# Performance work log

Measured on AMD Instinct MI355X. Metric: run time of the kernel, lower is better.

Reference implementation:

```python
import jax, jax.numpy as jnp
import numpy as np

BS, N, H = 8, 2048, 512
NEG_INF = -1.0e9
LEAKY_SLOPE = 0.01  # torch nn.LeakyReLU default


def setup_inputs() -> dict:
    key = jax.random.key(0)
    ks = jax.random.split(key, 8)
    feats = jax.random.normal(ks[0], (BS, N, H), dtype=jnp.float32)
    # random 0/1 adjacency with self-loops so every row has >=1 neighbor
    adj = jax.random.randint(ks[1], (BS, N, N), 0, 2).astype(jnp.float32)
    adj = jnp.maximum(adj, jnp.eye(N, dtype=jnp.float32)[None])
    s = 1.0 / np.sqrt(H)
    return {
        "feats": feats,
        "adj_mat": adj,
        "fc_w": jax.random.normal(ks[2], (H, H), dtype=jnp.float32) * s,
        "fc_b": jax.random.normal(ks[3], (H,), dtype=jnp.float32) * s,
        "q_w": jax.random.normal(ks[4], (1, H), dtype=jnp.float32) * s,
        "q_b": jax.random.normal(ks[5], (1,), dtype=jnp.float32) * s,
        "k_w": jax.random.normal(ks[6], (1, H), dtype=jnp.float32) * s,
        "k_b": jax.random.normal(ks[7], (1,), dtype=jnp.float32) * s,
    }


def reference(feats, adj_mat, fc_w, fc_b, q_w, q_b, k_w, k_b):
    # feats: [bs, N, H]; torch Linear: x @ W.T + b
    feat_proj = jnp.einsum("bnh,oh->bno", feats, fc_w) + fc_b          # [bs, N, H]
    q = jnp.einsum("bnh,oh->bno", feat_proj, q_w) + q_b                # [bs, N, 1]
    k = jnp.einsum("bnh,oh->bno", feat_proj, k_w) + k_b                # [bs, N, 1]
    logits = q + jnp.swapaxes(k, 2, 1)                                 # [bs, N, N] broadcast add
    masked = logits + (1.0 - adj_mat) * NEG_INF
    masked = jnp.where(masked >= 0, masked, LEAKY_SLOPE * masked)      # LeakyReLU
    atten = jax.nn.softmax(masked, axis=-1)
    # dropout is identity in eval mode
    out = jnp.einsum("bnm,bmh->bnh", atten, feat_proj)
    return out + feats  # residual=True
```

## Files before the change

kernel.cpp:

```cpp
#include <hip/hip_runtime.h>
#include <hip/hip_bf16.h>
#include <cstdint>
#include <cstddef>

#define BSZ 8
#define NN 2048
#define HH 512
#define MROWS (BSZ * NN)
#define LOG2E 1.44269504088896f

typedef __attribute__((ext_vector_type(4))) float f32x4;
typedef __attribute__((ext_vector_type(8))) short short8;
typedef __attribute__((ext_vector_type(4))) unsigned short us4;
typedef __attribute__((ext_vector_type(4))) uint32_t u32x4;

#if __has_builtin(__builtin_amdgcn_exp2f)
#define EXP2(x) __builtin_amdgcn_exp2f(x)
#else
#define EXP2(x) __expf((x) * 0.69314718056f)
#endif

static __device__ __forceinline__ unsigned short f2bf(float f) {
    uint32_t u = __builtin_bit_cast(uint32_t, f);
    u += 0x7fffu + ((u >> 16) & 1u);
    return (unsigned short)(u >> 16);
}

static __device__ __forceinline__ void async16(const unsigned short* g, unsigned short* l) {
    __builtin_amdgcn_global_load_lds(
        (const __attribute__((address_space(1))) void*)g,
        (__attribute__((address_space(3))) void*)l, 16, 0, 0);
}

__global__ __launch_bounds__(256) void prep_kernel(
    const float* __restrict__ feats, const float* __restrict__ fc_w,
    unsigned short* __restrict__ feats_bf, unsigned short* __restrict__ fcw_bf) {
    const int bid = blockIdx.x;
    const int tid = threadIdx.x;
    if (bid < 2048) {
        const int base = bid * 1024 + tid;
#pragma unroll
        for (int j = 0; j < 4; ++j) {
            const int i = base + j * 256;
            f32x4 v = ((const f32x4*)feats)[i];
            us4 o;
#pragma unroll
            for (int c = 0; c < 4; ++c) o[c] = f2bf(v[c]);
            ((us4*)feats_bf)[i] = o;
        }
    } else {
        const int base = (bid - 2048) * 1024 + tid;
#pragma unroll
        for (int j = 0; j < 4; ++j) {
            const int i = base + j * 256;
            f32x4 v = ((const f32x4*)fc_w)[i];
            us4 o;
#pragma unroll
            for (int c = 0; c < 4; ++c) o[c] = f2bf(v[c]);
            ((us4*)fcw_bf)[i] = o;
        }
    }
}

__global__ __launch_bounds__(256) void k2_kernel(
    const unsigned short* __restrict__ A, const unsigned short* __restrict__ Bt,
    const float* __restrict__ fc_b, const float* __restrict__ q_w,
    const float* __restrict__ k_w, const float* __restrict__ adj,
    unsigned short* __restrict__ fpT, unsigned char* __restrict__ maskb,
    float* __restrict__ qpart, float* __restrict__ kpart) {
    const int bid = blockIdx.x;
    const int tid = threadIdx.x;
    if (bid < 512) {
        __shared__ alignas(16) unsigned short As[128 * 32];
        __shared__ alignas(16) unsigned short Bs[128 * 32];
        __shared__ float qred[2][128], kred[2][128];
        const int wave = tid >> 6, lane = tid & 63;
        const int wi = wave >> 1, wj = wave & 1;
        const int n0 = (bid & 3) * 128;
        const int i0 = (bid >> 2) * 128;
        const int K = HH;
        const int lrow = lane >> 2;
        const int lseg = (lane & 3) * 8;
        const int fro = (lane & 15) * 32 + (lane >> 4) * 8;
        f32x4 acc[4][4];
#pragma unroll
        for (int a = 0; a < 4; ++a)
#pragma unroll
            for (int c = 0; c < 4; ++c) acc[a][c] = (f32x4)(0.f);

        for (int k0 = 0; k0 < K; k0 += 32) {
            __syncthreads();
            {
                const int c0 = wave * 2;
                const unsigned short* ga = A + (size_t)(i0 + c0 * 16 + lrow) * K + k0 + lseg;
                async16(ga, &As[(c0 * 16) * 32]);
                async16(ga + (size_t)16 * K, &As[(c0 * 16 + 16) * 32]);
                const unsigned short* gb = Bt + (size_t)(n0 + c0 * 16 + lrow) * K + k0 + lseg;
                async16(gb, &Bs[(c0 * 16) * 32]);
                async16(gb + (size_t)16 * K, &Bs[(c0 * 16 + 16) * 32]);
            }
            __syncthreads();
            short8 af[4], bf[4];
#pragma unroll
            for (int t = 0; t < 4; ++t) af[t] = *(const short8*)&As[(wi * 64 + t * 16) * 32 + fro];
#pragma unroll
            for (int t = 0; t < 4; ++t) bf[t] = *(const short8*)&Bs[(wj * 64 + t * 16) * 32 + fro];
#pragma unroll
            for (int it = 0; it < 4; ++it)
#pragma unroll
                for (int jt = 0; jt < 4; ++jt)
                    acc[it][jt] = __builtin_amdgcn_mfma_f32_16x16x32_bf16(af[it], bf[jt], acc[it][jt], 0, 0, 0);
        }

        int colv[4]; float cbv[4], qwv[4], kwv[4];
#pragma unroll
        for (int jt = 0; jt < 4; ++jt) {
            colv[jt] = n0 + wj * 64 + jt * 16 + (lane & 15);
            cbv[jt] = fc_b[colv[jt]];
            qwv[jt] = q_w[colv[jt]];
            kwv[jt] = k_w[colv[jt]];
        }
        const int b = i0 >> 11;
        const int il = i0 & 2047;
#pragma unroll
        for (int jt = 0; jt < 4; ++jt) {
#pragma unroll
            for (int it = 0; it < 4; ++it) {
                const int rb = wi * 64 + it * 16 + ((lane >> 4) << 2);
                us4 o;
#pragma unroll
                for (int r = 0; r < 4; ++r) o[r] = f2bf(acc[it][jt][r] + cbv[jt]);
                *(us4*)(fpT + ((size_t)b * HH + colv[jt]) * NN + il + rb) = o;
            }
        }
#pragma unroll
        for (int it = 0; it < 4; ++it) {
#pragma unroll
            for (int r = 0; r < 4; ++r) {
                float pq = 0.f, pk = 0.f;
#pragma unroll
                for (int jt = 0; jt < 4; ++jt) {
                    float v = acc[it][jt][r] + cbv[jt];
                    pq += v * qwv[jt];
                    pk += v * kwv[jt];
                }
                for (int off = 1; off < 16; off <<= 1) {
                    pq += __shfl_xor(pq, off, 64);
                    pk += __shfl_xor(pk, off, 64);
                }
                if ((lane & 15) == 0) {
                    const int rr = wi * 64 + it * 16 + ((lane >> 4) << 2) + r;
                    qred[wj][rr] = pq;
                    kred[wj][rr] = pk;
                }
            }
        }
        __syncthreads();
        if (tid < 128) {
            const size_t o = (size_t)(n0 >> 7) * MROWS + i0 + tid;
            qpart[o] = qred[0][tid] + qred[1][tid];
            kpart[o] = kred[0][tid] + kred[1][tid];
        }
    } else {
        const int a = bid - 512;
        const int wave = tid >> 6, lane = tid & 63;
#pragma unroll
        for (int s = 0; s < 2; ++s) {
            const int row = a * 8 + s * 4 + wave;
            const float* ar = adj + (size_t)row * NN;
#pragma unroll
            for (int p = 0; p < 4; ++p) {
                f32x4 v0 = *(const f32x4*)&ar[p * 512 + lane * 8];
                f32x4 v1 = *(const f32x4*)&ar[p * 512 + lane * 8 + 4];
                float fb = v0[0] + 2.f * v0[1] + 4.f * v0[2] + 8.f * v0[3]
                         + 16.f * v1[0] + 32.f * v1[1] + 64.f * v1[2] + 128.f * v1[3];
                maskb[(size_t)row * 256 + p * 64 + lane] = (unsigned char)(unsigned int)fb;
            }
        }
    }
}

__global__ __launch_bounds__(256) void fused_pv_kernel(
    const unsigned short* __restrict__ fpT, const unsigned char* __restrict__ maskb,
    const float* __restrict__ qpart, const float* __restrict__ kpart,
    const float* __restrict__ q_b, const float* __restrict__ k_b,
    const float* __restrict__ feats, float* __restrict__ out) {
    __shared__ alignas(16) unsigned short As[2][64 * 32];
    __shared__ alignas(16) unsigned short Bs[2][256 * 32];
    __shared__ float kLDS[NN];
    __shared__ float qLDS[64];
    __shared__ float rzl[64];
    const int tid = threadIdx.x;
    const int wave = tid >> 6, lane = tid & 63;
    const int wi = wave >> 1, wj = wave & 1;
    const int bid = blockIdx.x;
    const int b = bid & 7;
    const int t6 = bid >> 3;
    const int i0 = (t6 >> 1) * 64;
    const int n0 = (t6 & 1) * 256;
    const size_t rowbase = (size_t)b * NN + i0;

    {
        const float kb = k_b[0], qb = q_b[0];
#pragma unroll
        for (int s = 0; s < 8; ++s) {
            const int j = s * 256 + tid;
            const size_t gj = (size_t)b * NN + j;
            kLDS[j] = (kpart[gj] + kpart[MROWS + gj] + kpart[2 * MROWS + gj]
                     + kpart[3 * MROWS + gj] + kb) * LOG2E;
        }
        if (tid < 64) {
            const size_t gi = rowbase + tid;
            qLDS[tid] = (qpart[gi] + qpart[MROWS + gi] + qpart[2 * MROWS + gi]
                       + qpart[3 * MROWS + gi] + qb) * LOG2E;
        }
    }
    __syncthreads();

    const int r0 = tid >> 2;
    const int c8 = (tid & 3) * 8;
    const float qi = qLDS[r0];

    const unsigned short* Bt = fpT + (size_t)b * HH * NN;
    const uint32_t* mk = (const uint32_t*)maskb;
    const size_t mrow = (rowbase + r0) * 64;
    const int lrow = lane >> 2, lseg = (lane & 3) * 8;
    const int fro = (lane & 15) * 32 + (lane >> 4) * 8;

    auto stageB = [&](int buf, int k0) {
        const int rbase = wave * 64;
        const unsigned short* gb = Bt + (size_t)(n0 + rbase + lrow) * NN + k0 + lseg;
        async16(gb, &Bs[buf][rbase * 32]);
        async16(gb + (size_t)16 * NN, &Bs[buf][(rbase + 16) * 32]);
        async16(gb + (size_t)32 * NN, &Bs[buf][(rbase + 32) * 32]);
        async16(gb + (size_t)48 * NN, &Bs[buf][(rbase + 48) * 32]);
    };
    auto transform = [&](int buf, int k0, uint32_t mbits) {
        const f32x4 kv0 = *(const f32x4*)&kLDS[k0 + c8];
        const f32x4 kv1 = *(const f32x4*)&kLDS[k0 + c8 + 4];
        const uint32_t byte8 = (mbits >> c8) & 0xffu;
        float wv[8];
#pragma unroll
        for (int c = 0; c < 8; ++c) {
            float s = qi + (c < 4 ? kv0[c] : kv1[c - 4]);
            s = fmaxf(s, 0.01f * s);
            const float e = EXP2(s);
            wv[c] = ((byte8 >> c) & 1u) ? e : 0.f;
        }
        u32x4 pk;
#pragma unroll
        for (int p = 0; p < 4; ++p) {
            const uint32_t lo = __builtin_bit_cast(uint32_t, wv[2 * p]);
            const uint32_t hi = __builtin_bit_cast(uint32_t, wv[2 * p + 1]);
            pk[p] = __builtin_amdgcn_perm(hi, lo, 0x07060302u);
        }
        *(u32x4*)&As[buf][r0 * 32 + c8] = pk;
    };

    f32x4 acc[2][8];
#pragma unroll
    for (int a = 0; a < 2; ++a)
#pragma unroll
        for (int c = 0; c < 8; ++c) acc[a][c] = (f32x4)(0.f);
    f32x4 acc_z[2] = {(f32x4)(0.f), (f32x4)(0.f)};
    short8 ones;
#pragma unroll
    for (int j = 0; j < 8; ++j) ones[j] = (short)0x3F80;

    stageB(0, 0);
    transform(0, 0, mk[mrow]);
    uint32_t mnext = mk[mrow + 1];
    __syncthreads();

    for (int k0 = 0; k0 < NN; k0 += 32) {
        const int p = (k0 >> 5) & 1;
        if (k0 + 32 < NN) {
            stageB(p ^ 1, k0 + 32);
            uint32_t mfar = 0;
            if (k0 + 64 < NN) mfar = mk[mrow + ((k0 + 64) >> 5)];
            transform(p ^ 1, k0 + 32, mnext);
            mnext = mfar;
        }
        short8 af[2], bf[8];
#pragma unroll
        for (int t = 0; t < 2; ++t) af[t] = *(const short8*)&As[p][(wi * 32 + t * 16) * 32 + fro];
#pragma unroll
        for (int t = 0; t < 8; ++t) bf[t] = *(const short8*)&Bs[p][(wj * 128 + t * 16) * 32 + fro];
#pragma unroll
        for (int it = 0; it < 2; ++it)
#pragma unroll
            for (int jt = 0; jt < 8; ++jt)
                acc[it][jt] = __builtin_amdgcn_mfma_f32_16x16x32_bf16(af[it], bf[jt], acc[it][jt], 0, 0, 0);
        if (wj == 0) {
#pragma unroll
            for (int it = 0; it < 2; ++it)
                acc_z[it] = __builtin_amdgcn_mfma_f32_16x16x32_bf16(af[it], ones, acc_z[it], 0, 0, 0);
        }
        __syncthreads();
    }

    if (wj == 0 && (lane & 15) == 0) {
#pragma unroll
        for (int it = 0; it < 2; ++it) {
            const int rb = wi * 32 + it * 16 + ((lane >> 4) << 2);
#pragma unroll
            for (int r = 0; r < 4; ++r) rzl[rb + r] = 1.0f / acc_z[it][r];
        }
    }
    __syncthreads();

#pragma unroll
    for (int it = 0; it < 2; ++it) {
        const int rb = wi * 32 + it * 16 + ((lane >> 4) << 2);
        float rv[4];
#pragma unroll
        for (int r = 0; r < 4; ++r) rv[r] = rzl[rb + r];
#pragma unroll
        for (int jt = 0; jt < 8; ++jt) {
            const int col = n0 + wj * 128 + jt * 16 + (lane & 15);
#pragma unroll
            for (int r = 0; r < 4; ++r) {
                const size_t idx = (rowbase + rb + r) * HH + col;
                out[idx] = acc[it][jt][r] * rv[r] + feats[idx];
            }
        }
    }
}

extern "C" void kernel_launch(void* const* d_in, const int* in_sizes, int n_in,
                              void* d_out, int out_size, void* d_ws, size_t ws_size,
                              hipStream_t stream) {
    const float* feats = (const float*)d_in[0];
    const float* adj   = (const float*)d_in[1];
    const float* fc_w  = (const float*)d_in[2];
    const float* fc_b  = (const float*)d_in[3];
    const float* q_w   = (const float*)d_in[4];
    const float* q_b   = (const float*)d_in[5];
    const float* k_w   = (const float*)d_in[6];
    const float* k_b   = (const float*)d_in[7];
    float* out = (float*)d_out;

    char* w = (char*)d_ws;
    auto alloc = [&](size_t bytes) {
        char* p = w;
        w += (bytes + 255) & ~(size_t)255;
        return p;
    };
    unsigned short* feats_bf = (unsigned short*)alloc((size_t)BSZ * NN * HH * 2);
    unsigned short* fcw_bf   = (unsigned short*)alloc((size_t)HH * HH * 2);
    unsigned short* fpT   = (unsigned short*)alloc((size_t)BSZ * HH * NN * 2);
    unsigned char*  maskb = (unsigned char*)alloc((size_t)MROWS * 256);
    float* qpart = (float*)alloc((size_t)4 * MROWS * 4);
    float* kpart = (float*)alloc((size_t)4 * MROWS * 4);

    prep_kernel<<<2112, 256, 0, stream>>>(feats, fc_w, feats_bf, fcw_bf);
    k2_kernel<<<512 + 2048, 256, 0, stream>>>(feats_bf, fcw_bf, fc_b, q_w, k_w, adj,
                                              fpT, maskb, qpart, kpart);
    fused_pv_kernel<<<512, 256, 0, stream>>>(
        fpT, maskb, qpart, kpart, q_b, k_b, feats, out);
}
```

Measured before the change: 313.1 us.

## Move adjacency bitpacking into prep kernel and double-buffer projection GEMM loads

```diff
diff --git a/kernel.cpp b/kernel.cpp
--- a/kernel.cpp
+++ b/kernel.cpp
@@ -34,7 +34,9 @@
 
 __global__ __launch_bounds__(256) void prep_kernel(
     const float* __restrict__ feats, const float* __restrict__ fc_w,
-    unsigned short* __restrict__ feats_bf, unsigned short* __restrict__ fcw_bf) {
+    const float* __restrict__ adj,
+    unsigned short* __restrict__ feats_bf, unsigned short* __restrict__ fcw_bf,
+    unsigned char* __restrict__ maskb) {
     const int bid = blockIdx.x;
     const int tid = threadIdx.x;
     if (bid < 2048) {
@@ -48,7 +50,7 @@
             for (int c = 0; c < 4; ++c) o[c] = f2bf(v[c]);
             ((us4*)feats_bf)[i] = o;
         }
-    } else {
+    } else if (bid < 2112) {
         const int base = (bid - 2048) * 1024 + tid;
 #pragma unroll
         for (int j = 0; j < 4; ++j) {
@@ -59,110 +61,8 @@
             for (int c = 0; c < 4; ++c) o[c] = f2bf(v[c]);
             ((us4*)fcw_bf)[i] = o;
         }
-    }
-}
-
-__global__ __launch_bounds__(256) void k2_kernel(
-    const unsigned short* __restrict__ A, const unsigned short* __restrict__ Bt,
-    const float* __restrict__ fc_b, const float* __restrict__ q_w,
-    const float* __restrict__ k_w, const float* __restrict__ adj,
-    unsigned short* __restrict__ fpT, unsigned char* __restrict__ maskb,
-    float* __restrict__ qpart, float* __restrict__ kpart) {
-    const int bid = blockIdx.x;
-    const int tid = threadIdx.x;
-    if (bid < 512) {
-        __shared__ alignas(16) unsigned short As[128 * 32];
-        __shared__ alignas(16) unsigned short Bs[128 * 32];
-        __shared__ float qred[2][128], kred[2][128];
-        const int wave = tid >> 6, lane = tid & 63;
-        const int wi = wave >> 1, wj = wave & 1;
-        const int n0 = (bid & 3) * 128;
-        const int i0 = (bid >> 2) * 128;
-        const int K = HH;
-        const int lrow = lane >> 2;
-        const int lseg = (lane & 3) * 8;
-        const int fro = (lane & 15) * 32 + (lane >> 4) * 8;
-        f32x4 acc[4][4];
-#pragma unroll
-        for (int a = 0; a < 4; ++a)
-#pragma unroll
-            for (int c = 0; c < 4; ++c) acc[a][c] = (f32x4)(0.f);
-
-        for (int k0 = 0; k0 < K; k0 += 32) {
-            __syncthreads();
-            {
-                const int c0 = wave * 2;
-                const unsigned short* ga = A + (size_t)(i0 + c0 * 16 + lrow) * K + k0 + lseg;
-                async16(ga, &As[(c0 * 16) * 32]);
-                async16(ga + (size_t)16 * K, &As[(c0 * 16 + 16) * 32]);
-                const unsigned short* gb = Bt + (size_t)(n0 + c0 * 16 + lrow) * K + k0 + lseg;
-                async16(gb, &Bs[(c0 * 16) * 32]);
-                async16(gb + (size_t)16 * K, &Bs[(c0 * 16 + 16) * 32]);
-            }
-            __syncthreads();
-            short8 af[4], bf[4];
-#pragma unroll
-            for (int t = 0; t < 4; ++t) af[t] = *(const short8*)&As[(wi * 64 + t * 16) * 32 + fro];
-#pragma unroll
-            for (int t = 0; t < 4; ++t) bf[t] = *(const short8*)&Bs[(wj * 64 + t * 16) * 32 + fro];
-#pragma unroll
-            for (int it = 0; it < 4; ++it)
-#pragma unroll
-                for (int jt = 0; jt < 4; ++jt)
-                    acc[it][jt] = __builtin_amdgcn_mfma_f32_16x16x32_bf16(af[it], bf[jt], acc[it][jt], 0, 0, 0);
-        }
-
-        int colv[4]; float cbv[4], qwv[4], kwv[4];
-#pragma unroll
-        for (int jt = 0; jt < 4; ++jt) {
-            colv[jt] = n0 + wj * 64 + jt * 16 + (lane & 15);
-            cbv[jt] = fc_b[colv[jt]];
-            qwv[jt] = q_w[colv[jt]];
-            kwv[jt] = k_w[colv[jt]];
-        }
-        const int b = i0 >> 11;
-        const int il = i0 & 2047;
-#pragma unroll
-        for (int jt = 0; jt < 4; ++jt) {
-#pragma unroll
-            for (int it = 0; it < 4; ++it) {
-                const int rb = wi * 64 + it * 16 + ((lane >> 4) << 2);
-                us4 o;
-#pragma unroll
-                for (int r = 0; r < 4; ++r) o[r] = f2bf(acc[it][jt][r] + cbv[jt]);
-                *(us4*)(fpT + ((size_t)b * HH + colv[jt]) * NN + il + rb) = o;
-            }
-        }
-#pragma unroll
-        for (int it = 0; it < 4; ++it) {
-#pragma unroll
-            for (int r = 0; r < 4; ++r) {
-                float pq = 0.f, pk = 0.f;
-#pragma unroll
-                for (int jt = 0; jt < 4; ++jt) {
-                    float v = acc[it][jt][r] + cbv[jt];
-                    pq += v * qwv[jt];
-                    pk += v * kwv[jt];
-                }
-                for (int off = 1; off < 16; off <<= 1) {
-                    pq += __shfl_xor(pq, off, 64);
-                    pk += __shfl_xor(pk, off, 64);
-                }
-                if ((lane & 15) == 0) {
-                    const int rr = wi * 64 + it * 16 + ((lane >> 4) << 2) + r;
-                    qred[wj][rr] = pq;
-                    kred[wj][rr] = pk;
-                }
-            }
-        }
-        __syncthreads();
-        if (tid < 128) {
-            const size_t o = (size_t)(n0 >> 7) * MROWS + i0 + tid;
-            qpart[o] = qred[0][tid] + qred[1][tid];
-            kpart[o] = kred[0][tid] + kred[1][tid];
-        }
     } else {
-        const int a = bid - 512;
+        const int a = bid - 2112;
         const int wave = tid >> 6, lane = tid & 63;
 #pragma unroll
         for (int s = 0; s < 2; ++s) {
@@ -177,6 +77,111 @@
                 maskb[(size_t)row * 256 + p * 64 + lane] = (unsigned char)(unsigned int)fb;
             }
         }
+    }
+}
+
+__global__ __launch_bounds__(256) void k2_kernel(
+    const unsigned short* __restrict__ A, const unsigned short* __restrict__ Bt,
+    const float* __restrict__ fc_b, const float* __restrict__ q_w,
+    const float* __restrict__ k_w,
+    unsigned short* __restrict__ fpT,
+    float* __restrict__ qpart, float* __restrict__ kpart) {
+    __shared__ alignas(16) unsigned short As[2][128 * 32];
+    __shared__ alignas(16) unsigned short Bs[2][128 * 32];
+    __shared__ float qred[2][128], kred[2][128];
+    const int bid = blockIdx.x;
+    const int tid = threadIdx.x;
+    const int wave = tid >> 6, lane = tid & 63;
+    const int wi = wave >> 1, wj = wave & 1;
+    const int n0 = (bid & 3) * 128;
+    const int i0 = (bid >> 2) * 128;
+    const int K = HH;
+    const int lrow = lane >> 2;
+    const int lseg = (lane & 3) * 8;
+    const int fro = (lane & 15) * 32 + (lane >> 4) * 8;
+    f32x4 acc[4][4];
+#pragma unroll
+    for (int a = 0; a < 4; ++a)
+#pragma unroll
+        for (int c = 0; c < 4; ++c) acc[a][c] = (f32x4)(0.f);
+
+    auto stage = [&](int buf, int k0) {
+        const int c0 = wave * 2;
+        const unsigned short* ga = A + (size_t)(i0 + c0 * 16 + lrow) * K + k0 + lseg;
+        async16(ga, &As[buf][(c0 * 16) * 32]);
+        async16(ga + (size_t)16 * K, &As[buf][(c0 * 16 + 16) * 32]);
+        const unsigned short* gb = Bt + (size_t)(n0 + c0 * 16 + lrow) * K + k0 + lseg;
+        async16(gb, &Bs[buf][(c0 * 16) * 32]);
+        async16(gb + (size_t)16 * K, &Bs[buf][(c0 * 16 + 16) * 32]);
+    };
+
+    stage(0, 0);
+    __syncthreads();
+
+    for (int k0 = 0; k0 < K; k0 += 32) {
+        const int p = (k0 >> 5) & 1;
+        if (k0 + 32 < K) stage(p ^ 1, k0 + 32);
+        short8 af[4], bf[4];
+#pragma unroll
+        for (int t = 0; t < 4; ++t) af[t] = *(const short8*)&As[p][(wi * 64 + t * 16) * 32 + fro];
+#pragma unroll
+        for (int t = 0; t < 4; ++t) bf[t] = *(const short8*)&Bs[p][(wj * 64 + t * 16) * 32 + fro];
+#pragma unroll
+        for (int it = 0; it < 4; ++it)
+#pragma unroll
+            for (int jt = 0; jt < 4; ++jt)
+                acc[it][jt] = __builtin_amdgcn_mfma_f32_16x16x32_bf16(af[it], bf[jt], acc[it][jt], 0, 0, 0);
+        __syncthreads();
+    }
+
+    int colv[4]; float cbv[4], qwv[4], kwv[4];
+#pragma unroll
+    for (int jt = 0; jt < 4; ++jt) {
+        colv[jt] = n0 + wj * 64 + jt * 16 + (lane & 15);
+        cbv[jt] = fc_b[colv[jt]];
+        qwv[jt] = q_w[colv[jt]];
+        kwv[jt] = k_w[colv[jt]];
+    }
+    const int b = i0 >> 11;
+    const int il = i0 & 2047;
+#pragma unroll
+    for (int jt = 0; jt < 4; ++jt) {
+#pragma unroll
+        for (int it = 0; it < 4; ++it) {
+            const int rb = wi * 64 + it * 16 + ((lane >> 4) << 2);
+            us4 o;
+#pragma unroll
+            for (int r = 0; r < 4; ++r) o[r] = f2bf(acc[it][jt][r] + cbv[jt]);
+            *(us4*)(fpT + ((size_t)b * HH + colv[jt]) * NN + il + rb) = o;
+        }
+    }
+#pragma unroll
+    for (int it = 0; it < 4; ++it) {
+#pragma unroll
+        for (int r = 0; r < 4; ++r) {
+            float pq = 0.f, pk = 0.f;
+#pragma unroll
+            for (int jt = 0; jt < 4; ++jt) {
+                float v = acc[it][jt][r] + cbv[jt];
+                pq += v * qwv[jt];
+                pk += v * kwv[jt];
+            }
+            for (int off = 1; off < 16; off <<= 1) {
+                pq += __shfl_xor(pq, off, 64);
+                pk += __shfl_xor(pk, off, 64);
+            }
+            if ((lane & 15) == 0) {
+                const int rr = wi * 64 + it * 16 + ((lane >> 4) << 2) + r;
+                qred[wj][rr] = pq;
+                kred[wj][rr] = pk;
+            }
+        }
+    }
+    __syncthreads();
+    if (tid < 128) {
+        const size_t o = (size_t)(n0 >> 7) * MROWS + i0 + tid;
+        qpart[o] = qred[0][tid] + qred[1][tid];
+        kpart[o] = kred[0][tid] + kred[1][tid];
     }
 }
 
@@ -353,9 +358,9 @@
     float* qpart = (float*)alloc((size_t)4 * MROWS * 4);
     float* kpart = (float*)alloc((size_t)4 * MROWS * 4);
 
-    prep_kernel<<<2112, 256, 0, stream>>>(feats, fc_w, feats_bf, fcw_bf);
-    k2_kernel<<<512 + 2048, 256, 0, stream>>>(feats_bf, fcw_bf, fc_b, q_w, k_w, adj,
-                                              fpT, maskb, qpart, kpart);
+    prep_kernel<<<4160, 256, 0, stream>>>(feats, fc_w, adj, feats_bf, fcw_bf, maskb);
+    k2_kernel<<<512, 256, 0, stream>>>(feats_bf, fcw_bf, fc_b, q_w, k_w,
+                                       fpT, qpart, kpart);
     fused_pv_kernel<<<512, 256, 0, stream>>>(
         fpT, maskb, qpart, kpart, q_b, k_b, feats, out);
 }
```

Measured after the change: 314.1 us. About the same (+0.3%).

## Triple-buffer attention PV loop, double-buffer projection GEMM, interleave mask blocks

Applied to the files above, without the earlier changes.

```diff
diff --git a/kernel.cpp b/kernel.cpp
--- a/kernel.cpp
+++ b/kernel.cpp
@@ -68,48 +68,52 @@
     const float* __restrict__ k_w, const float* __restrict__ adj,
     unsigned short* __restrict__ fpT, unsigned char* __restrict__ maskb,
     float* __restrict__ qpart, float* __restrict__ kpart) {
+    __shared__ alignas(16) unsigned short As[2][64 * 32];
+    __shared__ alignas(16) unsigned short Bs[2][128 * 32];
+    __shared__ float qred[2][64], kred[2][64];
     const int bid = blockIdx.x;
     const int tid = threadIdx.x;
-    if (bid < 512) {
-        __shared__ alignas(16) unsigned short As[128 * 32];
-        __shared__ alignas(16) unsigned short Bs[128 * 32];
-        __shared__ float qred[2][128], kred[2][128];
-        const int wave = tid >> 6, lane = tid & 63;
+    const int wave = tid >> 6, lane = tid & 63;
+    if (bid % 3 == 0) {
+        const int g = bid / 3;
         const int wi = wave >> 1, wj = wave & 1;
-        const int n0 = (bid & 3) * 128;
-        const int i0 = (bid >> 2) * 128;
+        const int n0 = (g & 3) * 128;
+        const int i0 = (g >> 2) * 64;
         const int K = HH;
         const int lrow = lane >> 2;
         const int lseg = (lane & 3) * 8;
         const int fro = (lane & 15) * 32 + (lane >> 4) * 8;
-        f32x4 acc[4][4];
-#pragma unroll
-        for (int a = 0; a < 4; ++a)
+        f32x4 acc[2][4];
+#pragma unroll
+        for (int a = 0; a < 2; ++a)
 #pragma unroll
             for (int c = 0; c < 4; ++c) acc[a][c] = (f32x4)(0.f);
 
+        auto stage = [&](int buf, int k0) {
+            const unsigned short* ga = A + (size_t)(i0 + wave * 16 + lrow) * K + k0 + lseg;
+            async16(ga, &As[buf][(wave * 16) * 32]);
+            const unsigned short* gb = Bt + (size_t)(n0 + wave * 32 + lrow) * K + k0 + lseg;
+            async16(gb, &Bs[buf][(wave * 32) * 32]);
+            async16(gb + (size_t)16 * K, &Bs[buf][(wave * 32 + 16) * 32]);
+        };
+
+        stage(0, 0);
+        __syncthreads();
+
         for (int k0 = 0; k0 < K; k0 += 32) {
-            __syncthreads();
-            {
-                const int c0 = wave * 2;
-                const unsigned short* ga = A + (size_t)(i0 + c0 * 16 + lrow) * K + k0 + lseg;
-                async16(ga, &As[(c0 * 16) * 32]);
-                async16(ga + (size_t)16 * K, &As[(c0 * 16 + 16) * 32]);
-                const unsigned short* gb = Bt + (size_t)(n0 + c0 * 16 + lrow) * K + k0 + lseg;
-                async16(gb, &Bs[(c0 * 16) * 32]);
-                async16(gb + (size_t)16 * K, &Bs[(c0 * 16 + 16) * 32]);
-            }
-            __syncthreads();
-            short8 af[4], bf[4];
-#pragma unroll
-            for (int t = 0; t < 4; ++t) af[t] = *(const short8*)&As[(wi * 64 + t * 16) * 32 + fro];
-#pragma unroll
-            for (int t = 0; t < 4; ++t) bf[t] = *(const short8*)&Bs[(wj * 64 + t * 16) * 32 + fro];
-#pragma unroll
-            for (int it = 0; it < 4; ++it)
+            const int p = (k0 >> 5) & 1;
+            if (k0 + 32 < K) stage(p ^ 1, k0 + 32);
+            short8 af[2], bf[4];
+#pragma unroll
+            for (int t = 0; t < 2; ++t) af[t] = *(const short8*)&As[p][(wi * 32 + t * 16) * 32 + fro];
+#pragma unroll
+            for (int t = 0; t < 4; ++t) bf[t] = *(const short8*)&Bs[p][(wj * 64 + t * 16) * 32 + fro];
+#pragma unroll
+            for (int it = 0; it < 2; ++it)
 #pragma unroll
                 for (int jt = 0; jt < 4; ++jt)
                     acc[it][jt] = __builtin_amdgcn_mfma_f32_16x16x32_bf16(af[it], bf[jt], acc[it][jt], 0, 0, 0);
+            __syncthreads();
         }
 
         int colv[4]; float cbv[4], qwv[4], kwv[4];
@@ -125,8 +129,8 @@
 #pragma unroll
         for (int jt = 0; jt < 4; ++jt) {
 #pragma unroll
-            for (int it = 0; it < 4; ++it) {
-                const int rb = wi * 64 + it * 16 + ((lane >> 4) << 2);
+            for (int it = 0; it < 2; ++it) {
+                const int rb = wi * 32 + it * 16 + ((lane >> 4) << 2);
                 us4 o;
 #pragma unroll
                 for (int r = 0; r < 4; ++r) o[r] = f2bf(acc[it][jt][r] + cbv[jt]);
@@ -134,7 +138,7 @@
             }
         }
 #pragma unroll
-        for (int it = 0; it < 4; ++it) {
+        for (int it = 0; it < 2; ++it) {
 #pragma unroll
             for (int r = 0; r < 4; ++r) {
                 float pq = 0.f, pk = 0.f;
@@ -149,21 +153,20 @@
                     pk += __shfl_xor(pk, off, 64);
                 }
                 if ((lane & 15) == 0) {
-                    const int rr = wi * 64 + it * 16 + ((lane >> 4) << 2) + r;
+                    const int rr = wi * 32 + it * 16 + ((lane >> 4) << 2) + r;
                     qred[wj][rr] = pq;
                     kred[wj][rr] = pk;
                 }
             }
         }
         __syncthreads();
-        if (tid < 128) {
+        if (tid < 64) {
             const size_t o = (size_t)(n0 >> 7) * MROWS + i0 + tid;
             qpart[o] = qred[0][tid] + qred[1][tid];
             kpart[o] = kred[0][tid] + kred[1][tid];
         }
     } else {
-        const int a = bid - 512;
-        const int wave = tid >> 6, lane = tid & 63;
+        const int a = (bid / 3) * 2 + (bid % 3) - 1;
 #pragma unroll
         for (int s = 0; s < 2; ++s) {
             const int row = a * 8 + s * 4 + wave;
@@ -185,8 +188,8 @@
     const float* __restrict__ qpart, const float* __restrict__ kpart,
     const float* __restrict__ q_b, const float* __restrict__ k_b,
     const float* __restrict__ feats, float* __restrict__ out) {
-    __shared__ alignas(16) unsigned short As[2][64 * 32];
-    __shared__ alignas(16) unsigned short Bs[2][256 * 32];
+    __shared__ alignas(16) unsigned short As[3][64 * 32];
+    __shared__ alignas(16) unsigned short Bs[3][256 * 32];
     __shared__ float kLDS[NN];
     __shared__ float qLDS[64];
     __shared__ float rzl[64];
@@ -267,25 +270,13 @@
 #pragma unroll
     for (int j = 0; j < 8; ++j) ones[j] = (short)0x3F80;
 
-    stageB(0, 0);
-    transform(0, 0, mk[mrow]);
-    uint32_t mnext = mk[mrow + 1];
-    __syncthreads();
-
-    for (int k0 = 0; k0 < NN; k0 += 32) {
-        const int p = (k0 >> 5) & 1;
-        if (k0 + 32 < NN) {
-            stageB(p ^ 1, k0 + 32);
-            uint32_t mfar = 0;
-            if (k0 + 64 < NN) mfar = mk[mrow + ((k0 + 64) >> 5)];
-            transform(p ^ 1, k0 + 32, mnext);
-            mnext = mfar;
-        }
+    auto compute = [&](int rd) {
         short8 af[2], bf[8];
 #pragma unroll
-        for (int t = 0; t < 2; ++t) af[t] = *(const short8*)&As[p][(wi * 32 + t * 16) * 32 + fro];
-#pragma unroll
-        for (int t = 0; t < 8; ++t) bf[t] = *(const short8*)&Bs[p][(wj * 128 + t * 16) * 32 + fro];
+        for (int t = 0; t < 2; ++t) af[t] = *(const short8*)&As[rd][(wi * 32 + t * 16) * 32 + fro];
+#pragma unroll
+        for (int t = 0; t < 8; ++t) bf[t] = *(const short8*)&Bs[rd][(wj * 128 + t * 16) * 32 + fro];
+        __builtin_amdgcn_s_setprio(1);
 #pragma unroll
         for (int it = 0; it < 2; ++it)
 #pragma unroll
@@ -296,7 +287,58 @@
             for (int it = 0; it < 2; ++it)
                 acc_z[it] = __builtin_amdgcn_mfma_f32_16x16x32_bf16(af[it], ones, acc_z[it], 0, 0, 0);
         }
-        __syncthreads();
+        __builtin_amdgcn_s_setprio(0);
+    };
+
+    uint32_t mw_cur = mk[mrow];
+    uint32_t mw_nxt = mk[mrow + 1];
+    stageB(0, 0);
+    transform(0, 0, mw_cur);
+    asm volatile("s_waitcnt vmcnt(0)" ::: "memory");
+    __builtin_amdgcn_sched_barrier(0);
+    asm volatile("s_waitcnt lgkmcnt(0)" ::: "memory");
+    __builtin_amdgcn_s_barrier();
+    __builtin_amdgcn_sched_barrier(0);
+
+    for (int j = 0; j < 62; ++j) {
+        const int k0 = j * 32;
+        const int rd = j % 3, st = (j + 1) % 3;
+        uint32_t mnn;
+        {
+            const uint32_t* ma = mk + mrow + j + 2;
+            asm volatile("global_load_dword %0, %1, off"
+                         : "=v"(mnn) : "v"(ma) : "memory");
+        }
+        stageB(st, k0 + 32);
+        asm volatile("s_waitcnt vmcnt(5)" ::: "memory");
+        __builtin_amdgcn_sched_barrier(0);
+        transform(st, k0 + 32, mw_nxt);
+        mw_nxt = mnn;
+        asm volatile("s_waitcnt lgkmcnt(0)" ::: "memory");
+        __builtin_amdgcn_sched_barrier(0);
+        __builtin_amdgcn_s_barrier();
+        __builtin_amdgcn_sched_barrier(0);
+        compute(rd);
+    }
+    {
+        const int k0 = 62 * 32;
+        stageB(0, k0 + 32);
+        asm volatile("s_waitcnt vmcnt(4)" ::: "memory");
+        __builtin_amdgcn_sched_barrier(0);
+        transform(0, k0 + 32, mw_nxt);
+        asm volatile("s_waitcnt lgkmcnt(0)" ::: "memory");
+        __builtin_amdgcn_sched_barrier(0);
+        __builtin_amdgcn_s_barrier();
+        __builtin_amdgcn_sched_barrier(0);
+        compute(62 % 3);
+    }
+    {
+        asm volatile("s_waitcnt vmcnt(0)" ::: "memory");
+        __builtin_amdgcn_sched_barrier(0);
+        asm volatile("s_waitcnt lgkmcnt(0)" ::: "memory");
+        __builtin_amdgcn_s_barrier();
+        __builtin_amdgcn_sched_barrier(0);
+        compute(0);
     }
 
     if (wj == 0 && (lane & 15) == 0) {
@@ -354,8 +396,8 @@
     float* kpart = (float*)alloc((size_t)4 * MROWS * 4);
 
     prep_kernel<<<2112, 256, 0, stream>>>(feats, fc_w, feats_bf, fcw_bf);
-    k2_kernel<<<512 + 2048, 256, 0, stream>>>(feats_bf, fcw_bf, fc_b, q_w, k_w, adj,
-                                              fpT, maskb, qpart, kpart);
+    k2_kernel<<<3072, 256, 0, stream>>>(feats_bf, fcw_bf, fc_b, q_w, k_w, adj,
+                                        fpT, maskb, qpart, kpart);
     fused_pv_kernel<<<512, 256, 0, stream>>>(
         fpT, maskb, qpart, kpart, q_b, k_b, feats, out);
 }
```

Result: faster. 304.3 us (-2.8%).
